# Optimization experiments

Hardware: AMD Instinct MI355X
Metric: run time of the kernel (lower is better)

## Reference

```python
import jax, jax.numpy as jnp
import numpy as np

N, TQ, T = 32, 1, 8192
CQ, CK, U = 256, 256, 128


def setup_inputs() -> dict:
    key = jax.random.key(0)
    ks = jax.random.split(key, 8)
    query = jax.random.normal(ks[0], (N, TQ, CQ), dtype=jnp.float32)
    k = jax.random.normal(ks[1], (N, T, CK), dtype=jnp.float32)
    w_conv = jax.random.normal(ks[2], (CQ, CQ), dtype=jnp.float32) * (1.0 / np.sqrt(CQ))
    w_q = jax.random.normal(ks[3], (CQ, U), dtype=jnp.float32) * (1.0 / np.sqrt(CQ))
    w_k = jax.random.normal(ks[4], (CK, U), dtype=jnp.float32) * (1.0 / np.sqrt(CK))
    v = jax.random.normal(ks[5], (U,), dtype=jnp.float32) * (1.0 / np.sqrt(U))
    b = jnp.zeros((1, 1, U), dtype=jnp.float32)
    # pre-sampled Gumbel(0,1) noise for gumbel_softmax (tau=1, soft)
    u = jax.random.uniform(ks[6], (N, TQ, T), dtype=jnp.float32, minval=1e-6, maxval=1.0 - 1e-6)
    gumbel = -jnp.log(-jnp.log(u))
    return {"query": query, "key": k, "w_conv": w_conv, "w_q": w_q,
            "w_k": w_k, "v": v, "b": b, "gumbel": gumbel}


def reference(query, key, w_conv, w_q, w_k, v, b, gumbel):
    # Conv1d with kernel=stride=1, no bias == pointwise channel projection
    q = jnp.einsum('nlc,oc->nlo', query, w_conv)          # (N, 1, CQ)
    qp = jnp.einsum('nlc,cu->nlu', q, w_q)                # (N, 1, U)
    kp = jnp.einsum('ntc,cu->ntu', key, w_k)              # (N, T, U)
    # additive (Bahdanau) score: v^T tanh(q + k + b) -> (N, 1, T)
    score = jnp.einsum('ntu,u->nt', jnp.tanh(qp + kp + b), v)[:, None, :]
    # gumbel-softmax, tau=1, soft
    align = jax.nn.softmax(score + gumbel, axis=-1)       # (N, 1, T)
    context = jnp.einsum('nqt,ntc->nqc', align, key)      # (N, 1, CK)
    return (context, align)
```

## Files before the change

kernel.cpp:

```cpp
#include <hip/hip_runtime.h>
#include <hip/hip_bf16.h>

#define NB 32
#define T_LEN 8192
#define CKC 256
#define UQ 128
#define NBLK_PER_N 16
#define BLOCK_ROWS 512
#define NWIN 16
#define WIN_ROWS 32
#define PART_STRIDE 258
#define FIXED_MAX 25.0f

typedef short short8 __attribute__((ext_vector_type(8)));
typedef float f32x4 __attribute__((ext_vector_type(4)));
typedef unsigned short ushort4_t __attribute__((ext_vector_type(4)));

__device__ __forceinline__ unsigned short f2bf(float x) {
  union { float f; unsigned u; } un; un.f = x;
  unsigned r = un.u + 0x7FFFu + ((un.u >> 16) & 1u);
  return (unsigned short)(r >> 16);
}
__device__ __forceinline__ float bf2f(unsigned short h) {
  union { unsigned u; float f; } un; un.u = ((unsigned)h) << 16;
  return un.f;
}
__device__ __forceinline__ float fast_tanh(float x) {
  float e = __expf(2.0f * x);
  return 1.0f - 2.0f / (e + 1.0f);
}
__device__ __forceinline__ ushort4_t pack_bf16x4(f32x4 x) {
  union { __hip_bfloat162 h; unsigned short u[2]; } a, b;
  a.h = __float22bfloat162_rn(make_float2(x[0], x[1]));
  b.h = __float22bfloat162_rn(make_float2(x[2], x[3]));
  ushort4_t r; r[0] = a.u[0]; r[1] = a.u[1]; r[2] = b.u[0]; r[3] = b.u[1];
  return r;
}
__device__ __forceinline__ void barrier_lgkm() {
  asm volatile("s_waitcnt lgkmcnt(0)" ::: "memory");
  __builtin_amdgcn_s_barrier();
}
template <int N>
__device__ __forceinline__ float row_shl_add(float x) {
  int y = __builtin_amdgcn_update_dpp(0, __float_as_int(x),
                                      0x100 | N, 0xf, 0xf, true);
  return x + __int_as_float(y);
}
__device__ __forceinline__ float hsum4(f32x4 x) {
  return (x[0] + x[1]) + (x[2] + x[3]);
}

__global__ void prep_kernel(const float* __restrict__ query,
                            const float* __restrict__ w_conv,
                            const float* __restrict__ w_q,
                            const float* __restrict__ bvec,
                            const float* __restrict__ w_k,
                            float* __restrict__ qpb,
                            unsigned short* __restrict__ wkT_hi) {
  const int tid = threadIdx.x;
  if (blockIdx.x >= NB) {
    const int c = blockIdx.x - NB;
    if (tid < UQ) wkT_hi[tid * CKC + c] = f2bf(w_k[c * UQ + tid]);
    return;
  }
  __shared__ float qr[256];
  __shared__ float qv[256];
  const int n = blockIdx.x;
  qr[tid] = query[n * 256 + tid];
  __syncthreads();
  float acc = 0.f;
  const f32x4* wrow = (const f32x4*)(w_conv + (size_t)tid * 256);
  const f32x4* q4 = (const f32x4*)qr;
#pragma unroll 8
  for (int i = 0; i < 64; ++i) {
    f32x4 wv4 = wrow[i];
    f32x4 qq = q4[i];
    acc += wv4[0] * qq[0] + wv4[1] * qq[1] + wv4[2] * qq[2] + wv4[3] * qq[3];
  }
  qv[tid] = acc;
  __syncthreads();
  if (tid < UQ) {
    float a2 = bvec[tid];
#pragma unroll 4
    for (int c = 0; c < 256; ++c) a2 += qv[c] * w_q[c * UQ + tid];
    qpb[n * UQ + tid] = a2;
  }
}

__global__ __launch_bounds__(512, 2)
void fused_attn_kernel(const float* __restrict__ key,
                       const float* __restrict__ gumbel,
                       const float* __restrict__ v,
                       const float* __restrict__ qpb,
                       const unsigned short* __restrict__ wkT_hi,
                       float* __restrict__ part,
                       float* __restrict__ out_align) {
  __shared__ __align__(16) unsigned short bufHi[3][2][16 * CKC];
  __shared__ __align__(16) float spart_t[2][WIN_ROWS][4];
  __shared__ __align__(16) float ctx4[4][256];
  __shared__ float gbuf[BLOCK_ROWS];
  __shared__ float lred[4];

  const int tid = threadIdx.x;
  const int lane = tid & 63;
  const int wv = tid >> 6;
  const int bid = blockIdx.x;
  const int n = bid >> 4;
  const int blk = bid & 15;
  const int t0 = blk * BLOCK_ROWS;

  gbuf[tid] = gumbel[n * T_LEN + t0 + tid];

  const float* keyN = key + (size_t)n * T_LEN * CKC;

  if (wv >= 4) {
    const int cw = wv - 4;
    const int ul = lane & 15;
    const int u0 = 32 * cw + ul;
    const int u1 = u0 + 16;
    const float qpb0 = qpb[n * UQ + u0];
    const float qpb1 = qpb[n * UQ + u1];
    const float v0 = v[u0];
    const float v1 = v[u1];
    short8 bh0[8], bh1[8];
    {
      const int koff = (lane >> 4) * 8;
#pragma unroll
      for (int kt = 0; kt < 8; ++kt) {
        bh0[kt] = *(const short8*)(wkT_hi + (size_t)u0 * CKC + kt * 32 + koff);
        bh1[kt] = *(const short8*)(wkT_hi + (size_t)u1 * CKC + kt * 32 + koff);
      }
    }
    const unsigned axor = ((unsigned)(ul & 7)) << 4;
    const unsigned abase = (unsigned)(ul * 512 + (lane >> 4) * 16);

    barrier_lgkm();

    int pc = 0, ps = 0;
    for (int pr = 0; pr < NWIN; ++pr) {
#pragma unroll
      for (int tl = 0; tl < 2; ++tl) {
        const char* base = (const char*)&bufHi[pc][tl][0];
        f32x4 acc0 = {qpb0, qpb0, qpb0, qpb0};
        f32x4 acc1 = {qpb1, qpb1, qpb1, qpb1};
        __builtin_amdgcn_s_setprio(1);
#pragma unroll
        for (int kt = 0; kt < 8; ++kt) {
          short8 kf = *(const short8*)(base + ((abase + (unsigned)(kt * 64)) ^ axor));
          acc0 = __builtin_amdgcn_mfma_f32_16x16x32_bf16(kf, bh0[kt], acc0, 0, 0, 0);
          acc1 = __builtin_amdgcn_mfma_f32_16x16x32_bf16(kf, bh1[kt], acc1, 0, 0, 0);
        }
        __builtin_amdgcn_s_setprio(0);
        float svt[4];
#pragma unroll
        for (int i = 0; i < 4; ++i)
          svt[i] = v0 * fast_tanh(acc0[i]) + v1 * fast_tanh(acc1[i]);
#pragma unroll
        for (int i = 0; i < 4; ++i) {
          svt[i] = row_shl_add<8>(svt[i]);
          svt[i] = row_shl_add<4>(svt[i]);
          svt[i] = row_shl_add<2>(svt[i]);
          svt[i] = row_shl_add<1>(svt[i]);
        }
        if (ul == 0) {
          const int g4 = lane >> 4;
#pragma unroll
          for (int i = 0; i < 4; ++i)
            spart_t[ps][tl * 16 + g4 * 4 + i][cw] = svt[i];
        }
      }
      barrier_lgkm();
      pc = (pc == 2) ? 0 : pc + 1;
      ps ^= 1;
    }
    barrier_lgkm();
  } else {
    const int pw = wv;
    unsigned ldsoff[8];
    int rl_of[8];
#pragma unroll
    for (int j = 0; j < 8; ++j) {
      const int rl = j * 4 + pw;
      rl_of[j] = rl;
      const int tl = rl >> 4;
      const unsigned rloc = (unsigned)(rl & 15);
      ldsoff[j] = (unsigned)(tl * 8192) +
                  (((rloc * 512u) + (unsigned)(lane * 8)) ^ ((rloc & 7u) << 4));
    }
    f32x4 stg[8];
#pragma unroll
    for (int j = 0; j < 8; ++j)
      stg[j] = *(const f32x4*)(keyN + (size_t)(t0 + rl_of[j]) * CKC + lane * 4);
#pragma unroll
    for (int j = 0; j < 8; ++j)
      *(ushort4_t*)((char*)&bufHi[0][0][0] + ldsoff[j]) = pack_bf16x4(stg[j]);
#pragma unroll
    for (int j = 0; j < 8; ++j)
      stg[j] = *(const f32x4*)(keyN + (size_t)(t0 + WIN_ROWS + rl_of[j]) * CKC + lane * 4);

    barrier_lgkm();

    float l_acc = 0.f;
    f32x4 ctx = {0.f, 0.f, 0.f, 0.f};
    int pnext = 1;
    int pprev = 2;
    int qs = 1;
    for (int pr = 0; pr < NWIN; ++pr) {
      if (pr + 1 < NWIN) {
#pragma unroll
        for (int j = 0; j < 8; ++j)
          *(ushort4_t*)((char*)&bufHi[pnext][0][0] + ldsoff[j]) = pack_bf16x4(stg[j]);
      }
      if (pr + 2 < NWIN) {
        const int tb = t0 + (pr + 2) * WIN_ROWS;
#pragma unroll
        for (int j = 0; j < 8; ++j)
          stg[j] = *(const f32x4*)(keyN + (size_t)(tb + rl_of[j]) * CKC + lane * 4);
      }
      if (pr > 0) {
        const int rwin = (pr - 1) * WIN_ROWS;
#pragma unroll
        for (int k = 0; k < 8; ++k) {
          const int rl = k * 4 + pw;
          const f32x4 sp = *(const f32x4*)&spart_t[qs][rl][0];
          float st = gbuf[rwin + rl] + hsum4(sp);
          float w = __expf(st - FIXED_MAX);
          const int tl = rl >> 4;
          const unsigned rloc = (unsigned)(rl & 15);
          const unsigned ro = (((rloc * 512u) + (unsigned)(lane * 8)) ^ ((rloc & 7u) << 4));
          ushort4_t rv = *(const ushort4_t*)((const char*)&bufHi[pprev][tl][0] + ro);
#pragma unroll
          for (int j2 = 0; j2 < 4; ++j2) ctx[j2] += w * bf2f(rv[j2]);
          l_acc += w;
          if (lane == 0) out_align[(size_t)n * T_LEN + t0 + rwin + rl] = st;
        }
      }
      barrier_lgkm();
      pprev = (pprev == 2) ? 0 : pprev + 1;
      pnext = (pnext == 2) ? 0 : pnext + 1;
      qs ^= 1;
    }
    {
      const int q2 = (NWIN - 1) & 1;
      const int pc2 = (NWIN - 1) % 3;
      const int rwin = (NWIN - 1) * WIN_ROWS;
#pragma unroll
      for (int k = 0; k < 8; ++k) {
        const int rl = k * 4 + pw;
        const f32x4 sp = *(const f32x4*)&spart_t[q2][rl][0];
        float st = gbuf[rwin + rl] + hsum4(sp);
        float w = __expf(st - FIXED_MAX);
        const int tl = rl >> 4;
        const unsigned rloc = (unsigned)(rl & 15);
        const unsigned ro = (((rloc * 512u) + (unsigned)(lane * 8)) ^ ((rloc & 7u) << 4));
        ushort4_t rv = *(const ushort4_t*)((const char*)&bufHi[pc2][tl][0] + ro);
#pragma unroll
        for (int j2 = 0; j2 < 4; ++j2) ctx[j2] += w * bf2f(rv[j2]);
        l_acc += w;
        if (lane == 0) out_align[(size_t)n * T_LEN + t0 + rwin + rl] = st;
      }
    }
    *(f32x4*)&ctx4[pw][lane * 4] = ctx;
    if (lane == 0) lred[pw] = l_acc;
    barrier_lgkm();
  }

  float* pb = part + (size_t)bid * PART_STRIDE;
  if (tid == 0)
    pb[0] = (lred[0] + lred[1]) + (lred[2] + lred[3]);
  if (tid < 256)
    pb[2 + tid] = (ctx4[0][tid] + ctx4[1][tid]) + (ctx4[2][tid] + ctx4[3][tid]);
}

__global__ void combine_kernel(const float* __restrict__ part,
                               float* __restrict__ out_ctx,
                               float* __restrict__ out_align) {
  __shared__ float lp[NBLK_PER_N];
  const int n = blockIdx.x >> 3;
  const int seg = blockIdx.x & 7;
  const int tid = threadIdx.x;
  if (tid < NBLK_PER_N)
    lp[tid] = part[(size_t)(n * NBLK_PER_N + tid) * PART_STRIDE];
  __syncthreads();
  float lg = 0.f;
#pragma unroll
  for (int j = 0; j < NBLK_PER_N; ++j) lg += lp[j];
  const float inv = 1.0f / lg;
  if (seg == 0) {
    float ca = 0.f;
#pragma unroll
    for (int j = 0; j < NBLK_PER_N; ++j)
      ca += part[(size_t)(n * NBLK_PER_N + j) * PART_STRIDE + 2 + tid];
    out_ctx[n * 256 + tid] = ca * inv;
  }
  const int tb = seg * (T_LEN / 8);
#pragma unroll
  for (int i = 0; i < T_LEN / 8 / 256; ++i) {
    const int t = tb + i * 256 + tid;
    float s = out_align[(size_t)n * T_LEN + t];
    out_align[(size_t)n * T_LEN + t] = __expf(s - FIXED_MAX) * inv;
  }
}

extern "C" void kernel_launch(void* const* d_in, const int* in_sizes, int n_in,
                              void* d_out, int out_size, void* d_ws, size_t ws_size,
                              hipStream_t stream) {
  const float* query = (const float*)d_in[0];
  const float* key = (const float*)d_in[1];
  const float* w_conv = (const float*)d_in[2];
  const float* w_q = (const float*)d_in[3];
  const float* w_k = (const float*)d_in[4];
  const float* v = (const float*)d_in[5];
  const float* b = (const float*)d_in[6];
  const float* gumbel = (const float*)d_in[7];

  float* out = (float*)d_out;
  float* out_ctx = out;
  float* out_align = out + NB * CKC;

  char* ws = (char*)d_ws;
  float* qpb = (float*)ws;
  unsigned short* wkT_hi = (unsigned short*)(ws + 16 * 1024);
  float* part = (float*)(ws + 144 * 1024);

  prep_kernel<<<dim3(NB + CKC), dim3(256), 0, stream>>>(
      query, w_conv, w_q, b, w_k, qpb, wkT_hi);
  fused_attn_kernel<<<dim3(NB * NBLK_PER_N), dim3(512), 0, stream>>>(
      key, gumbel, v, qpb, wkT_hi, part, out_align);
  combine_kernel<<<dim3(NB * 8), dim3(256), 0, stream>>>(part, out_ctx, out_align);
}
```

Before: 78.12 us.

## Process two windows per barrier with four-slot LDS ring buffer

The producer/consumer warp-specialized pipeline now handles two 32-row windows per barrier step instead of one. It uses a 4-slot LDS ring for the bf16 key tiles and score partials, and each producer wave keeps two staging register sets. This halves the number of block-wide barriers and doubles the global loads in flight per step. In exchange it raises LDS use (bufHi grows to 64KB) and register pressure, which could hurt occupancy at launch_bounds(512,2).

```diff
diff --git a/kernel.cpp b/kernel.cpp
--- a/kernel.cpp
+++ b/kernel.cpp
@@ -95,8 +95,8 @@
                        const unsigned short* __restrict__ wkT_hi,
                        float* __restrict__ part,
                        float* __restrict__ out_align) {
-  __shared__ __align__(16) unsigned short bufHi[3][2][16 * CKC];
-  __shared__ __align__(16) float spart_t[2][WIN_ROWS][4];
+  __shared__ __align__(16) unsigned short bufHi[4][2][16 * CKC];
+  __shared__ __align__(16) float spart_t[4][WIN_ROWS][4];
   __shared__ __align__(16) float ctx4[4][256];
   __shared__ float gbuf[BLOCK_ROWS];
   __shared__ float lred[4];
@@ -133,133 +133,135 @@
     }
     const unsigned axor = ((unsigned)(ul & 7)) << 4;
     const unsigned abase = (unsigned)(ul * 512 + (lane >> 4) * 16);
+    const int g4 = lane >> 4;
 
     barrier_lgkm();
 
-    int pc = 0, ps = 0;
-    for (int pr = 0; pr < NWIN; ++pr) {
-#pragma unroll
-      for (int tl = 0; tl < 2; ++tl) {
-        const char* base = (const char*)&bufHi[pc][tl][0];
-        f32x4 acc0 = {qpb0, qpb0, qpb0, qpb0};
-        f32x4 acc1 = {qpb1, qpb1, qpb1, qpb1};
-        __builtin_amdgcn_s_setprio(1);
-#pragma unroll
-        for (int kt = 0; kt < 8; ++kt) {
-          short8 kf = *(const short8*)(base + ((abase + (unsigned)(kt * 64)) ^ axor));
-          acc0 = __builtin_amdgcn_mfma_f32_16x16x32_bf16(kf, bh0[kt], acc0, 0, 0, 0);
-          acc1 = __builtin_amdgcn_mfma_f32_16x16x32_bf16(kf, bh1[kt], acc1, 0, 0, 0);
-        }
-        __builtin_amdgcn_s_setprio(0);
-        float svt[4];
-#pragma unroll
-        for (int i = 0; i < 4; ++i)
-          svt[i] = v0 * fast_tanh(acc0[i]) + v1 * fast_tanh(acc1[i]);
-#pragma unroll
-        for (int i = 0; i < 4; ++i) {
-          svt[i] = row_shl_add<8>(svt[i]);
-          svt[i] = row_shl_add<4>(svt[i]);
-          svt[i] = row_shl_add<2>(svt[i]);
-          svt[i] = row_shl_add<1>(svt[i]);
-        }
-        if (ul == 0) {
-          const int g4 = lane >> 4;
+    for (int k = 0; k < 8; ++k) {
+#pragma unroll
+      for (int hw = 0; hw < 2; ++hw) {
+        const int w = 2 * k + hw;
+        const int bi = w & 3;
+#pragma unroll
+        for (int tl = 0; tl < 2; ++tl) {
+          const char* base = (const char*)&bufHi[bi][tl][0];
+          f32x4 acc0 = {qpb0, qpb0, qpb0, qpb0};
+          f32x4 acc1 = {qpb1, qpb1, qpb1, qpb1};
+          __builtin_amdgcn_s_setprio(1);
+#pragma unroll
+          for (int kt = 0; kt < 8; ++kt) {
+            short8 kf = *(const short8*)(base + ((abase + (unsigned)(kt * 64)) ^ axor));
+            acc0 = __builtin_amdgcn_mfma_f32_16x16x32_bf16(kf, bh0[kt], acc0, 0, 0, 0);
+            acc1 = __builtin_amdgcn_mfma_f32_16x16x32_bf16(kf, bh1[kt], acc1, 0, 0, 0);
+          }
+          __builtin_amdgcn_s_setprio(0);
+          float svt[4];
 #pragma unroll
           for (int i = 0; i < 4; ++i)
-            spart_t[ps][tl * 16 + g4 * 4 + i][cw] = svt[i];
+            svt[i] = v0 * fast_tanh(acc0[i]) + v1 * fast_tanh(acc1[i]);
+#pragma unroll
+          for (int i = 0; i < 4; ++i) {
+            svt[i] = row_shl_add<8>(svt[i]);
+            svt[i] = row_shl_add<4>(svt[i]);
+            svt[i] = row_shl_add<2>(svt[i]);
+            svt[i] = row_shl_add<1>(svt[i]);
+          }
+          if (ul == 0) {
+#pragma unroll
+            for (int i = 0; i < 4; ++i)
+              spart_t[bi][tl * 16 + g4 * 4 + i][cw] = svt[i];
+          }
         }
       }
       barrier_lgkm();
-      pc = (pc == 2) ? 0 : pc + 1;
-      ps ^= 1;
     }
     barrier_lgkm();
   } else {
     const int pw = wv;
     unsigned ldsoff[8];
-    int rl_of[8];
 #pragma unroll
     for (int j = 0; j < 8; ++j) {
       const int rl = j * 4 + pw;
-      rl_of[j] = rl;
       const int tl = rl >> 4;
       const unsigned rloc = (unsigned)(rl & 15);
       ldsoff[j] = (unsigned)(tl * 8192) +
                   (((rloc * 512u) + (unsigned)(lane * 8)) ^ ((rloc & 7u) << 4));
     }
-    f32x4 stg[8];
-#pragma unroll
-    for (int j = 0; j < 8; ++j)
-      stg[j] = *(const f32x4*)(keyN + (size_t)(t0 + rl_of[j]) * CKC + lane * 4);
-#pragma unroll
-    for (int j = 0; j < 8; ++j)
-      *(ushort4_t*)((char*)&bufHi[0][0][0] + ldsoff[j]) = pack_bf16x4(stg[j]);
-#pragma unroll
-    for (int j = 0; j < 8; ++j)
-      stg[j] = *(const f32x4*)(keyN + (size_t)(t0 + WIN_ROWS + rl_of[j]) * CKC + lane * 4);
+    f32x4 stgA[8], stgB[8];
+#pragma unroll
+    for (int j = 0; j < 8; ++j) {
+      const int rl = j * 4 + pw;
+      stgA[j] = *(const f32x4*)(keyN + (size_t)(t0 + rl) * CKC + lane * 4);
+      stgB[j] = *(const f32x4*)(keyN + (size_t)(t0 + WIN_ROWS + rl) * CKC + lane * 4);
+    }
+#pragma unroll
+    for (int j = 0; j < 8; ++j) {
+      *(ushort4_t*)((char*)&bufHi[0][0][0] + ldsoff[j]) = pack_bf16x4(stgA[j]);
+      *(ushort4_t*)((char*)&bufHi[1][0][0] + ldsoff[j]) = pack_bf16x4(stgB[j]);
+    }
+#pragma unroll
+    for (int j = 0; j < 8; ++j) {
+      const int rl = j * 4 + pw;
+      stgA[j] = *(const f32x4*)(keyN + (size_t)(t0 + 2 * WIN_ROWS + rl) * CKC + lane * 4);
+      stgB[j] = *(const f32x4*)(keyN + (size_t)(t0 + 3 * WIN_ROWS + rl) * CKC + lane * 4);
+    }
 
     barrier_lgkm();
 
     float l_acc = 0.f;
     f32x4 ctx = {0.f, 0.f, 0.f, 0.f};
-    int pnext = 1;
-    int pprev = 2;
-    int qs = 1;
-    for (int pr = 0; pr < NWIN; ++pr) {
-      if (pr + 1 < NWIN) {
-#pragma unroll
-        for (int j = 0; j < 8; ++j)
-          *(ushort4_t*)((char*)&bufHi[pnext][0][0] + ldsoff[j]) = pack_bf16x4(stg[j]);
+
+#define SOFTMAX_WIN(W)                                                        \
+    {                                                                         \
+      const int bi = (W) & 3;                                                 \
+      const int rwin = (W) * WIN_ROWS;                                        \
+      _Pragma("unroll")                                                       \
+      for (int k2 = 0; k2 < 8; ++k2) {                                        \
+        const int rl = k2 * 4 + pw;                                           \
+        const f32x4 sp = *(const f32x4*)&spart_t[bi][rl][0];                  \
+        float st = gbuf[rwin + rl] + hsum4(sp);                               \
+        float wgt = __expf(st - FIXED_MAX);                                   \
+        const int tl = rl >> 4;                                               \
+        const unsigned rloc = (unsigned)(rl & 15);                            \
+        const unsigned ro = (((rloc * 512u) + (unsigned)(lane * 8)) ^         \
+                             ((rloc & 7u) << 4));                             \
+        ushort4_t rv = *(const ushort4_t*)((const char*)&bufHi[bi][tl][0] + ro); \
+        _Pragma("unroll")                                                     \
+        for (int j2 = 0; j2 < 4; ++j2) ctx[j2] += wgt * bf2f(rv[j2]);         \
+        l_acc += wgt;                                                         \
+        if (lane == 0) out_align[(size_t)n * T_LEN + t0 + rwin + rl] = st;    \
+      }                                                                       \
+    }
+
+    for (int k = 0; k < 8; ++k) {
+      if (k > 0) {
+        SOFTMAX_WIN(2 * k - 2);
+        SOFTMAX_WIN(2 * k - 1);
       }
-      if (pr + 2 < NWIN) {
-        const int tb = t0 + (pr + 2) * WIN_ROWS;
-#pragma unroll
-        for (int j = 0; j < 8; ++j)
-          stg[j] = *(const f32x4*)(keyN + (size_t)(tb + rl_of[j]) * CKC + lane * 4);
-      }
-      if (pr > 0) {
-        const int rwin = (pr - 1) * WIN_ROWS;
-#pragma unroll
-        for (int k = 0; k < 8; ++k) {
-          const int rl = k * 4 + pw;
-          const f32x4 sp = *(const f32x4*)&spart_t[qs][rl][0];
-          float st = gbuf[rwin + rl] + hsum4(sp);
-          float w = __expf(st - FIXED_MAX);
-          const int tl = rl >> 4;
-          const unsigned rloc = (unsigned)(rl & 15);
-          const unsigned ro = (((rloc * 512u) + (unsigned)(lane * 8)) ^ ((rloc & 7u) << 4));
-          ushort4_t rv = *(const ushort4_t*)((const char*)&bufHi[pprev][tl][0] + ro);
-#pragma unroll
-          for (int j2 = 0; j2 < 4; ++j2) ctx[j2] += w * bf2f(rv[j2]);
-          l_acc += w;
-          if (lane == 0) out_align[(size_t)n * T_LEN + t0 + rwin + rl] = st;
+      if (k < 7) {
+        const int biA = (2 * k + 2) & 3;
+        const int biB = (2 * k + 3) & 3;
+#pragma unroll
+        for (int j = 0; j < 8; ++j) {
+          *(ushort4_t*)((char*)&bufHi[biA][0][0] + ldsoff[j]) = pack_bf16x4(stgA[j]);
+          *(ushort4_t*)((char*)&bufHi[biB][0][0] + ldsoff[j]) = pack_bf16x4(stgB[j]);
+        }
+        if (k < 6) {
+          const int tbA = t0 + (2 * k + 4) * WIN_ROWS;
+          const int tbB = t0 + (2 * k + 5) * WIN_ROWS;
+#pragma unroll
+          for (int j = 0; j < 8; ++j) {
+            const int rl = j * 4 + pw;
+            stgA[j] = *(const f32x4*)(keyN + (size_t)(tbA + rl) * CKC + lane * 4);
+            stgB[j] = *(const f32x4*)(keyN + (size_t)(tbB + rl) * CKC + lane * 4);
+          }
         }
       }
       barrier_lgkm();
-      pprev = (pprev == 2) ? 0 : pprev + 1;
-      pnext = (pnext == 2) ? 0 : pnext + 1;
-      qs ^= 1;
-    }
-    {
-      const int q2 = (NWIN - 1) & 1;
-      const int pc2 = (NWIN - 1) % 3;
-      const int rwin = (NWIN - 1) * WIN_ROWS;
-#pragma unroll
-      for (int k = 0; k < 8; ++k) {
-        const int rl = k * 4 + pw;
-        const f32x4 sp = *(const f32x4*)&spart_t[q2][rl][0];
-        float st = gbuf[rwin + rl] + hsum4(sp);
-        float w = __expf(st - FIXED_MAX);
-        const int tl = rl >> 4;
-        const unsigned rloc = (unsigned)(rl & 15);
-        const unsigned ro = (((rloc * 512u) + (unsigned)(lane * 8)) ^ ((rloc & 7u) << 4));
-        ushort4_t rv = *(const ushort4_t*)((const char*)&bufHi[pc2][tl][0] + ro);
-#pragma unroll
-        for (int j2 = 0; j2 < 4; ++j2) ctx[j2] += w * bf2f(rv[j2]);
-        l_acc += w;
-        if (lane == 0) out_align[(size_t)n * T_LEN + t0 + rwin + rl] = st;
-      }
-    }
+    }
+    SOFTMAX_WIN(14);
+    SOFTMAX_WIN(15);
+#undef SOFTMAX_WIN
     *(f32x4*)&ctx4[pw][lane * 4] = ctx;
     if (lane == 0) lred[pw] = l_acc;
     barrier_lgkm();
```

Result: slower. 89.63 us (+14.7%).
